# Kernel optimization log

Measured on AMD Instinct MI355X. Metric: run time of the kernel, lower is better.

## Reference

```python
import jax, jax.numpy as jnp
import numpy as np

B, C, H, W = 8, 256, 64, 64   # batch, num_hiddens, spatial
N, D = 1024, 256              # n_embed, embedding_dim
TEMP = 1.0                    # temp_init


def setup_inputs() -> dict:
    key = jax.random.key(0)
    k1, k2, k3 = jax.random.split(key, 3)
    z = jax.random.normal(k1, (B, C, H, W), dtype=jnp.float32)
    # 1x1 conv == per-pixel linear: weight [n_embed, num_hiddens], bias [n_embed]
    proj_w = jax.random.normal(k2, (N, C), dtype=jnp.float32) * 0.02
    proj_b = jnp.zeros((N,), dtype=jnp.float32)
    embed = jax.random.normal(k3, (N, D), dtype=jnp.float32) * 0.02
    return {"z": z, "proj_w": proj_w, "proj_b": proj_b, "embed": embed}


def reference(z, proj_w, proj_b, embed):
    # logits = Conv2d(num_hiddens, n_embed, 1)(z)  -> [b, n, h, w]
    logits = jnp.einsum('bchw,nc->bnhw', z, proj_w) + proj_b[None, :, None, None]
    # argmax_softmax (straight-through) over the codebook axis (dim=1), tau=TEMP
    y_soft = jax.nn.softmax(logits / TEMP, axis=1)
    ind = jnp.argmax(y_soft, axis=1)  # [b, h, w]
    y_hard = jax.nn.one_hot(ind, N, axis=1, dtype=logits.dtype)  # [b, n, h, w]
    soft_one_hot = y_hard - jax.lax.stop_gradient(y_soft) + y_soft
    # z_q = einsum('b n h w, n d -> b d h w', soft_one_hot, embed)
    z_q = jnp.einsum('bnhw,nd->bdhw', soft_one_hot, embed)
    diff = jnp.zeros((1,), dtype=logits.dtype)
    return (z_q, diff, ind)
```

## Files before the change

kernel.cpp:

```cpp
#include <hip/hip_runtime.h>
#include <math.h>

#define HWP 4096
#define CCH 256
#define NN  1024
#define DD  256
#define ZQ_SIZE (8 * DD * HWP)
#define MARGIN 1e-4f
#define WLCAP 4096

typedef _Float16 h8 __attribute__((ext_vector_type(8)));
typedef float    f4 __attribute__((ext_vector_type(4)));

__global__ __launch_bounds__(256) void split_w_k(
    const float* __restrict__ w, _Float16* __restrict__ whS, _Float16* __restrict__ wlS,
    int* __restrict__ wcount)
{
    if (blockIdx.x == 0 && threadIdx.x == 0) *wcount = 0;
    const int t = blockIdx.x * 256 + threadIdx.x;
    const int l = t & 63;
    const int frag = t >> 6;
    const int kc = frag & 7, r16 = frag >> 3;
    const int row = r16 * 16 + (l & 15);
    const int c   = kc * 32 + (l >> 4) * 8;
    const float* src = w + (size_t)row * CCH + c;
    _Float16 hv[8], lv[8];
#pragma unroll
    for (int j = 0; j < 8; ++j) {
        const float x = src[j];
        const _Float16 h = (_Float16)x;
        hv[j] = h;
        lv[j] = (_Float16)(x - (float)h);
    }
    *(h8*)(whS + (size_t)t * 8) = *(const h8*)hv;
    *(h8*)(wlS + (size_t)t * 8) = *(const h8*)lv;
}

__global__ __launch_bounds__(512, 4) void mfma_gemm_k(
    const float* __restrict__ z,
    const _Float16* __restrict__ whS, const _Float16* __restrict__ wlS,
    const float* __restrict__ bias, const float* __restrict__ embed,
    int* __restrict__ wcount, int* __restrict__ wlist,
    float* __restrict__ out)
{
    __shared__ __align__(16) char smem[71680];
    __shared__ int indsh2[64];
    float* s_best = (float*)(smem + 65536);
    float* s_sec  = (float*)(smem + 67584);
    int*   s_idx  = (int*)  (smem + 69632);

    const int tid = threadIdx.x;
    const int l   = tid & 63;
    const int wv  = tid >> 6;
    const int mh  = wv >> 2;
    const int ng  = wv & 3;
    const int c15 = l & 15, g = l >> 4;
    const int pix0 = blockIdx.x * 64;
    const int b = pix0 >> 12, p0 = pix0 & 4095;

    {
        const int px = tid & 63;
        const int wv2 = tid >> 6;
        const int p16 = px >> 4;
        const float* zb = z + (size_t)b * CCH * HWP + p0 + px;
#pragma unroll
        for (int it = 0; it < 4; ++it) {
            const int cg = wv2 * 4 + it;
            const int c = cg * 8;
            float xv[8];
#pragma unroll
            for (int i = 0; i < 8; ++i) xv[i] = zb[(size_t)(c + i) * HWP];
            _Float16 hv[8], lv[8];
#pragma unroll
            for (int i = 0; i < 8; ++i) {
                const _Float16 h = (_Float16)xv[i];
                hv[i] = h;
                lv[i] = (_Float16)(xv[i] - (float)h);
            }
            const int kc = cg >> 2;
            const int lane = (px & 15) + 16 * (cg & 3);
            const int off = ((p16 * 8 + kc) * 64 + lane) * 16;
            *(h8*)(smem + off)         = *(const h8*)hv;
            *(h8*)(smem + 32768 + off) = *(const h8*)lv;
        }
    }
    __syncthreads();

    float best[8], sec[8]; int bidx[8];
#pragma unroll
    for (int s = 0; s < 8; ++s) { best[s] = -INFINITY; sec[s] = -INFINITY; bidx[s] = 0; }

#pragma unroll 1
    for (int nt = 0; nt < 4; ++nt) {
        const int n0 = nt * 256 + ng * 64;
        const int r16_0 = n0 >> 4;
        f4 acc[2][4];
#pragma unroll
        for (int mf = 0; mf < 2; ++mf)
#pragma unroll
            for (int nf = 0; nf < 4; ++nf) acc[mf][nf] = (f4)0.f;

#pragma unroll 2
        for (int kc = 0; kc < 8; ++kc) {
            h8 ah[2], al[2], bh[4], bl[4];
#pragma unroll
            for (int mf = 0; mf < 2; ++mf) {
                const int ao = (((mh * 2 + mf) * 8 + kc) * 64 + l) * 16;
                ah[mf] = *(const h8*)(smem + ao);
                al[mf] = *(const h8*)(smem + 32768 + ao);
            }
#pragma unroll
            for (int nf = 0; nf < 4; ++nf) {
                const size_t bo = (((size_t)(r16_0 + nf) * 8 + kc) * 64 + l) * 8;
                bh[nf] = *(const h8*)(whS + bo);
                bl[nf] = *(const h8*)(wlS + bo);
            }
#pragma unroll
            for (int mf = 0; mf < 2; ++mf)
#pragma unroll
                for (int nf = 0; nf < 4; ++nf) {
                    acc[mf][nf] = __builtin_amdgcn_mfma_f32_16x16x32_f16(ah[mf], bh[nf], acc[mf][nf], 0, 0, 0);
                    acc[mf][nf] = __builtin_amdgcn_mfma_f32_16x16x32_f16(ah[mf], bl[nf], acc[mf][nf], 0, 0, 0);
                    acc[mf][nf] = __builtin_amdgcn_mfma_f32_16x16x32_f16(al[mf], bh[nf], acc[mf][nf], 0, 0, 0);
                }
        }
#pragma unroll
        for (int nf = 0; nf < 4; ++nf) {
            const int n_abs = n0 + nf * 16 + c15;
            const float bv = bias[n_abs];
#pragma unroll
            for (int mf = 0; mf < 2; ++mf)
#pragma unroll
                for (int r = 0; r < 4; ++r) {
                    const float v = acc[mf][nf][r] + bv;
                    const int s = mf * 4 + r;
                    if (v > best[s]) { sec[s] = best[s]; best[s] = v; bidx[s] = n_abs; }
                    else if (v > sec[s]) sec[s] = v;
                }
        }
    }

#pragma unroll
    for (int d = 1; d < 16; d <<= 1) {
#pragma unroll
        for (int s = 0; s < 8; ++s) {
            const float ob = __shfl_xor(best[s], d, 64);
            const float os = __shfl_xor(sec[s], d, 64);
            const int   oi = __shfl_xor(bidx[s], d, 64);
            if (ob > best[s])       { sec[s] = fmaxf(best[s], os); best[s] = ob; bidx[s] = oi; }
            else if (ob == best[s]) { sec[s] = ob; bidx[s] = (oi < bidx[s]) ? oi : bidx[s]; }
            else                    { sec[s] = fmaxf(sec[s], ob); }
        }
    }
#pragma unroll
    for (int s = 0; s < 8; ++s) {
        if (c15 == s) {
            const int px = (mh * 2 + (s >> 2)) * 16 + g * 4 + (s & 3);
            s_best[wv * 64 + px] = best[s];
            s_sec [wv * 64 + px] = sec[s];
            s_idx [wv * 64 + px] = bidx[s];
        }
    }
    __syncthreads();
    if (tid < 64) {
        const int wb = (tid >> 5) * 4;
        float b0 = s_best[wb * 64 + tid], s0 = s_sec[wb * 64 + tid]; int i0 = s_idx[wb * 64 + tid];
#pragma unroll
        for (int c = 1; c < 4; ++c) {
            const float ob = s_best[(wb + c) * 64 + tid], os = s_sec[(wb + c) * 64 + tid];
            const int   oi = s_idx [(wb + c) * 64 + tid];
            if (ob > b0 || (ob == b0 && oi < i0)) { s0 = fmaxf(b0, os); b0 = ob; i0 = oi; }
            else                                  { s0 = fmaxf(s0, ob); }
        }
        const int pix = pix0 + tid;
        indsh2[tid] = i0;
        out[ZQ_SIZE + 1 + pix] = (float)i0;
        if (b0 - s0 < MARGIN) {
            const int pos = atomicAdd(wcount, 1);
            if (pos < WLCAP) wlist[pos] = pix;
        }
    }
    if (blockIdx.x == 0 && tid == 0) out[ZQ_SIZE] = 0.0f;
    __syncthreads();

    float (*tile)[257] = (float (*)[257])smem;
    const int lq = tid & 63, wq = tid >> 6;
    const int l32 = tid & 31, dq = tid >> 5;
#pragma unroll 1
    for (int pp = 0; pp < 2; ++pp) {
#pragma unroll
        for (int it = 0; it < 4; ++it) {
            const int pl = it * 8 + wq;
            const int row = indsh2[pp * 32 + pl];
            const float4 e = *(const float4*)(embed + (size_t)row * DD + lq * 4);
            tile[pl][lq * 4 + 0] = e.x;
            tile[pl][lq * 4 + 1] = e.y;
            tile[pl][lq * 4 + 2] = e.z;
            tile[pl][lq * 4 + 3] = e.w;
        }
        __syncthreads();
        float* outz = out + (size_t)b * DD * HWP + p0 + pp * 32;
#pragma unroll
        for (int dd = 0; dd < 16; ++dd) {
            const int d = dd * 16 + dq;
            outz[(size_t)d * HWP + l32] = tile[l32][d];
        }
        __syncthreads();
    }
}

__global__ __launch_bounds__(256) void fixup_k(
    const float* __restrict__ z, const float* __restrict__ w,
    const float* __restrict__ bias, const float* __restrict__ embed,
    const int* __restrict__ wcount, const int* __restrict__ wlist,
    float* __restrict__ out)
{
    __shared__ float zsh[256];
    __shared__ float m_v[4];
    __shared__ int   m_i[4];
    __shared__ int   s_i;

    const int tid = threadIdx.x;
    const int l = tid & 63, wv = tid >> 6;
    const int c15 = l & 15, q = l >> 4;
    int nw = *wcount;
    if (nw > WLCAP) nw = WLCAP;

    for (int e = blockIdx.x; e < nw; e += 256) {
        const int pix = wlist[e];
        const int b = pix >> 12, p = pix & 4095;
        __syncthreads();
        zsh[tid] = z[((size_t)b * CCH + tid) * HWP + p];
        __syncthreads();

        float best = -INFINITY; int bi = 0;
        for (int g16 = 0; g16 < 16; ++g16) {
            const int row = wv * 256 + g16 * 16 + c15;
            const float* wr = w + (size_t)row * CCH + q * 64;
            float part = 0.f;
#pragma unroll
            for (int j = 0; j < 16; ++j) {
                const float4 w4 = *(const float4*)(wr + j * 4);
                const float4 z4 = *(const float4*)&zsh[q * 64 + j * 4];
                part = fmaf(w4.x, z4.x, part);
                part = fmaf(w4.y, z4.y, part);
                part = fmaf(w4.z, z4.z, part);
                part = fmaf(w4.w, z4.w, part);
            }
            part += __shfl_xor(part, 16, 64);
            part += __shfl_xor(part, 32, 64);
            const float v = part + bias[row];
            if (v > best) { best = v; bi = row; }
        }
#pragma unroll
        for (int d = 1; d < 16; d <<= 1) {
            const float ob = __shfl_xor(best, d, 64);
            const int   oi = __shfl_xor(bi, d, 64);
            if (ob > best || (ob == best && oi < bi)) { best = ob; bi = oi; }
        }
        if (l == 0) { m_v[wv] = best; m_i[wv] = bi; }
        __syncthreads();
        if (tid == 0) {
            float v = m_v[0]; int i = m_i[0];
#pragma unroll
            for (int t = 1; t < 4; ++t)
                if (m_v[t] > v || (m_v[t] == v && m_i[t] < i)) { v = m_v[t]; i = m_i[t]; }
            s_i = i;
            out[ZQ_SIZE + 1 + pix] = (float)i;
        }
        __syncthreads();
        const int ii = s_i;
        out[((size_t)b * DD + tid) * HWP + p] = embed[(size_t)ii * DD + tid];
    }
}

extern "C" void kernel_launch(void* const* d_in, const int* in_sizes, int n_in,
                              void* d_out, int out_size, void* d_ws, size_t ws_size,
                              hipStream_t stream) {
    const float* z     = (const float*)d_in[0];
    const float* w     = (const float*)d_in[1];
    const float* bias  = (const float*)d_in[2];
    const float* embed = (const float*)d_in[3];
    float* out = (float*)d_out;

    _Float16* whS = (_Float16*)d_ws;
    _Float16* wlS = (_Float16*)((char*)d_ws + 524288);
    int* wcount = (int*)((char*)d_ws + 1048576);
    int* wlist  = (int*)((char*)d_ws + 1048832);

    hipLaunchKernelGGL(split_w_k,   dim3(128), dim3(256), 0, stream, w, whS, wlS, wcount);
    hipLaunchKernelGGL(mfma_gemm_k, dim3(512), dim3(512), 0, stream,
                       z, whS, wlS, bias, embed, wcount, wlist, out);
    hipLaunchKernelGGL(fixup_k,     dim3(256), dim3(256), 0, stream,
                       z, w, bias, embed, wcount, wlist, out);
}
```

Baseline: 180.9 us.

## Drop low-half weight MFMA term, widen fixup margin, batch fixup pixels

Removes the W-low correction term from the split-fp16 GEMM, so the main kernel issues two MFMAs per fragment instead of three and no longer loads or stores the low half of the weights. To compensate for the lower precision, the ambiguity margin grows from 1e-4 to 2e-3, which sends more pixels to the exact fp32 fixup pass. The fixup kernel now handles four pixels per block, reusing each weight load across them, and launches 512 blocks. The risk is that many more pixels need fixup, possibly overflowing the 4096-entry worklist cap, which would leave some argmax results inexact.

```diff
diff --git a/kernel.cpp b/kernel.cpp
--- a/kernel.cpp
+++ b/kernel.cpp
@@ -6,14 +6,14 @@
 #define NN  1024
 #define DD  256
 #define ZQ_SIZE (8 * DD * HWP)
-#define MARGIN 1e-4f
+#define MARGIN 2e-3f
 #define WLCAP 4096
 
 typedef _Float16 h8 __attribute__((ext_vector_type(8)));
 typedef float    f4 __attribute__((ext_vector_type(4)));
 
 __global__ __launch_bounds__(256) void split_w_k(
-    const float* __restrict__ w, _Float16* __restrict__ whS, _Float16* __restrict__ wlS,
+    const float* __restrict__ w, _Float16* __restrict__ whS,
     int* __restrict__ wcount)
 {
     if (blockIdx.x == 0 && threadIdx.x == 0) *wcount = 0;
@@ -24,21 +24,15 @@
     const int row = r16 * 16 + (l & 15);
     const int c   = kc * 32 + (l >> 4) * 8;
     const float* src = w + (size_t)row * CCH + c;
-    _Float16 hv[8], lv[8];
-#pragma unroll
-    for (int j = 0; j < 8; ++j) {
-        const float x = src[j];
-        const _Float16 h = (_Float16)x;
-        hv[j] = h;
-        lv[j] = (_Float16)(x - (float)h);
-    }
+    _Float16 hv[8];
+#pragma unroll
+    for (int j = 0; j < 8; ++j) hv[j] = (_Float16)src[j];
     *(h8*)(whS + (size_t)t * 8) = *(const h8*)hv;
-    *(h8*)(wlS + (size_t)t * 8) = *(const h8*)lv;
 }
 
 __global__ __launch_bounds__(512, 4) void mfma_gemm_k(
     const float* __restrict__ z,
-    const _Float16* __restrict__ whS, const _Float16* __restrict__ wlS,
+    const _Float16* __restrict__ whS,
     const float* __restrict__ bias, const float* __restrict__ embed,
     int* __restrict__ wcount, int* __restrict__ wlist,
     float* __restrict__ out)
@@ -102,7 +96,7 @@
 
 #pragma unroll 2
         for (int kc = 0; kc < 8; ++kc) {
-            h8 ah[2], al[2], bh[4], bl[4];
+            h8 ah[2], al[2], bh[4];
 #pragma unroll
             for (int mf = 0; mf < 2; ++mf) {
                 const int ao = (((mh * 2 + mf) * 8 + kc) * 64 + l) * 16;
@@ -113,14 +107,12 @@
             for (int nf = 0; nf < 4; ++nf) {
                 const size_t bo = (((size_t)(r16_0 + nf) * 8 + kc) * 64 + l) * 8;
                 bh[nf] = *(const h8*)(whS + bo);
-                bl[nf] = *(const h8*)(wlS + bo);
             }
 #pragma unroll
             for (int mf = 0; mf < 2; ++mf)
 #pragma unroll
                 for (int nf = 0; nf < 4; ++nf) {
                     acc[mf][nf] = __builtin_amdgcn_mfma_f32_16x16x32_f16(ah[mf], bh[nf], acc[mf][nf], 0, 0, 0);
-                    acc[mf][nf] = __builtin_amdgcn_mfma_f32_16x16x32_f16(ah[mf], bl[nf], acc[mf][nf], 0, 0, 0);
                     acc[mf][nf] = __builtin_amdgcn_mfma_f32_16x16x32_f16(al[mf], bh[nf], acc[mf][nf], 0, 0, 0);
                 }
         }
@@ -215,62 +207,95 @@
     const int* __restrict__ wcount, const int* __restrict__ wlist,
     float* __restrict__ out)
 {
-    __shared__ float zsh[256];
-    __shared__ float m_v[4];
-    __shared__ int   m_i[4];
-    __shared__ int   s_i;
+    __shared__ float zsh[4][256];
+    __shared__ float m_v[4][4];
+    __shared__ int   m_i[4][4];
+    __shared__ int   s_i[4];
 
     const int tid = threadIdx.x;
     const int l = tid & 63, wv = tid >> 6;
     const int c15 = l & 15, q = l >> 4;
     int nw = *wcount;
     if (nw > WLCAP) nw = WLCAP;
-
-    for (int e = blockIdx.x; e < nw; e += 256) {
-        const int pix = wlist[e];
-        const int b = pix >> 12, p = pix & 4095;
-        __syncthreads();
-        zsh[tid] = z[((size_t)b * CCH + tid) * HWP + p];
-        __syncthreads();
-
-        float best = -INFINITY; int bi = 0;
+    if (nw < 0) nw = 0;
+    const int ntask = (nw + 3) >> 2;
+
+    for (int t = blockIdx.x; t < ntask; t += 512) {
+        const int e0 = t * 4;
+        const int npx = (nw - e0 < 4) ? (nw - e0) : 4;
+        int pixv[4];
+#pragma unroll
+        for (int px = 0; px < 4; ++px) {
+            const int e = e0 + ((px < npx) ? px : (npx - 1));
+            pixv[px] = wlist[e];
+        }
+        __syncthreads();
+#pragma unroll
+        for (int px = 0; px < 4; ++px) {
+            const int pix = pixv[px];
+            const int b = pix >> 12, p = pix & 4095;
+            zsh[px][tid] = z[((size_t)b * CCH + tid) * HWP + p];
+        }
+        __syncthreads();
+
+        float best[4]; int bi[4];
+#pragma unroll
+        for (int px = 0; px < 4; ++px) { best[px] = -INFINITY; bi[px] = 0; }
+
         for (int g16 = 0; g16 < 16; ++g16) {
             const int row = wv * 256 + g16 * 16 + c15;
             const float* wr = w + (size_t)row * CCH + q * 64;
-            float part = 0.f;
+            float part[4] = {0.f, 0.f, 0.f, 0.f};
 #pragma unroll
             for (int j = 0; j < 16; ++j) {
                 const float4 w4 = *(const float4*)(wr + j * 4);
-                const float4 z4 = *(const float4*)&zsh[q * 64 + j * 4];
-                part = fmaf(w4.x, z4.x, part);
-                part = fmaf(w4.y, z4.y, part);
-                part = fmaf(w4.z, z4.z, part);
-                part = fmaf(w4.w, z4.w, part);
-            }
-            part += __shfl_xor(part, 16, 64);
-            part += __shfl_xor(part, 32, 64);
-            const float v = part + bias[row];
-            if (v > best) { best = v; bi = row; }
+#pragma unroll
+                for (int px = 0; px < 4; ++px) {
+                    const float4 z4 = *(const float4*)&zsh[px][q * 64 + j * 4];
+                    part[px] = fmaf(w4.x, z4.x, part[px]);
+                    part[px] = fmaf(w4.y, z4.y, part[px]);
+                    part[px] = fmaf(w4.z, z4.z, part[px]);
+                    part[px] = fmaf(w4.w, z4.w, part[px]);
+                }
+            }
+            const float bv = bias[row];
+#pragma unroll
+            for (int px = 0; px < 4; ++px) {
+                float pv = part[px];
+                pv += __shfl_xor(pv, 16, 64);
+                pv += __shfl_xor(pv, 32, 64);
+                const float v = pv + bv;
+                if (v > best[px]) { best[px] = v; bi[px] = row; }
+            }
         }
 #pragma unroll
         for (int d = 1; d < 16; d <<= 1) {
-            const float ob = __shfl_xor(best, d, 64);
-            const int   oi = __shfl_xor(bi, d, 64);
-            if (ob > best || (ob == best && oi < bi)) { best = ob; bi = oi; }
-        }
-        if (l == 0) { m_v[wv] = best; m_i[wv] = bi; }
-        __syncthreads();
-        if (tid == 0) {
-            float v = m_v[0]; int i = m_i[0];
-#pragma unroll
-            for (int t = 1; t < 4; ++t)
-                if (m_v[t] > v || (m_v[t] == v && m_i[t] < i)) { v = m_v[t]; i = m_i[t]; }
-            s_i = i;
-            out[ZQ_SIZE + 1 + pix] = (float)i;
-        }
-        __syncthreads();
-        const int ii = s_i;
-        out[((size_t)b * DD + tid) * HWP + p] = embed[(size_t)ii * DD + tid];
+#pragma unroll
+            for (int px = 0; px < 4; ++px) {
+                const float ob = __shfl_xor(best[px], d, 64);
+                const int   oi = __shfl_xor(bi[px], d, 64);
+                if (ob > best[px] || (ob == best[px] && oi < bi[px])) { best[px] = ob; bi[px] = oi; }
+            }
+        }
+        if (l == 0) {
+#pragma unroll
+            for (int px = 0; px < 4; ++px) { m_v[wv][px] = best[px]; m_i[wv][px] = bi[px]; }
+        }
+        __syncthreads();
+        if (tid < 4) {
+            float v = m_v[0][tid]; int i = m_i[0][tid];
+#pragma unroll
+            for (int t2 = 1; t2 < 4; ++t2)
+                if (m_v[t2][tid] > v || (m_v[t2][tid] == v && m_i[t2][tid] < i)) { v = m_v[t2][tid]; i = m_i[t2][tid]; }
+            s_i[tid] = i;
+            if (tid < npx) out[ZQ_SIZE + 1 + pixv[tid]] = (float)i;
+        }
+        __syncthreads();
+        for (int px = 0; px < npx; ++px) {
+            const int pix = pixv[px];
+            const int b = pix >> 12, p = pix & 4095;
+            out[((size_t)b * DD + tid) * HWP + p] = embed[(size_t)s_i[px] * DD + tid];
+        }
     }
 }
 
@@ -284,13 +309,12 @@
     float* out = (float*)d_out;
 
     _Float16* whS = (_Float16*)d_ws;
-    _Float16* wlS = (_Float16*)((char*)d_ws + 524288);
-    int* wcount = (int*)((char*)d_ws + 1048576);
-    int* wlist  = (int*)((char*)d_ws + 1048832);
-
-    hipLaunchKernelGGL(split_w_k,   dim3(128), dim3(256), 0, stream, w, whS, wlS, wcount);
+    int* wcount = (int*)((char*)d_ws + 524288);
+    int* wlist  = (int*)((char*)d_ws + 524544);
+
+    hipLaunchKernelGGL(split_w_k,   dim3(128), dim3(256), 0, stream, w, whS, wcount);
     hipLaunchKernelGGL(mfma_gemm_k, dim3(512), dim3(512), 0, stream,
-                       z, whS, wlS, bias, embed, wcount, wlist, out);
-    hipLaunchKernelGGL(fixup_k,     dim3(256), dim3(256), 0, stream,
+                       z, whS, bias, embed, wcount, wlist, out);
+    hipLaunchKernelGGL(fixup_k,     dim3(512), dim3(256), 0, stream,
                        z, w, bias, embed, wcount, wlist, out);
 }
```

Result: slower. 190.7 us (+5.4%).
